# Optimization experiments

Measured on AMD Instinct MI355X. Metric: run time of the kernel, lower is better.

The kernel has to match this reference:

```python
import jax, jax.numpy as jnp
import numpy as np

B, N, M = 4, 2048, 2048
DIM, DIM_KEYS, DIM_OUT = 512, 512, 512
HEADS, DIM_HEAD = 8, 64
INNER = HEADS * DIM_HEAD


def setup_inputs() -> dict:
    key = jax.random.key(0)
    ks = jax.random.split(key, 9)
    x = jax.random.normal(ks[0], (B, N, DIM), dtype=jnp.float32)
    context = jax.random.normal(ks[1], (B, M, DIM_KEYS), dtype=jnp.float32)
    mask = jax.random.randint(ks[2], (B, N), 0, 2).astype(bool)
    context_mask = jax.random.randint(ks[3], (B, M), 0, 2).astype(bool)
    Wq = jax.random.normal(ks[4], (DIM, INNER), dtype=jnp.float32) * 0.02
    Wkv = jax.random.normal(ks[5], (DIM_KEYS, 2 * INNER), dtype=jnp.float32) * 0.02
    Wo = jax.random.normal(ks[6], (INNER, DIM_OUT), dtype=jnp.float32) * 0.02
    bo = jnp.zeros((DIM_OUT,), dtype=jnp.float32)
    null_key = jax.random.normal(ks[7], (DIM_HEAD,), dtype=jnp.float32)
    null_value = jax.random.normal(ks[8], (DIM_HEAD,), dtype=jnp.float32)
    return {"x": x, "context": context, "mask": mask, "context_mask": context_mask,
            "Wq": Wq, "Wkv": Wkv, "Wo": Wo, "bo": bo,
            "null_key": null_key, "null_value": null_value}


def reference(x, context, mask, context_mask, Wq, Wkv, Wo, bo, null_key, null_value):
    b, n, _ = x.shape
    m = context.shape[1]
    h, dh = HEADS, DIM_HEAD
    scale = dh ** -0.5

    # projections -> [b, h, n, dh]
    q = (x @ Wq).reshape(b, n, h, dh).transpose(0, 2, 1, 3)
    kv = context @ Wkv  # [b, m, 2*inner]
    k, v = jnp.split(kv, 2, axis=-1)
    k = k.reshape(b, m, h, dh).transpose(0, 2, 1, 3)
    v = v.reshape(b, m, h, dh).transpose(0, 2, 1, 3)

    # prepend null key/value token -> j = m + 1
    nk = jnp.broadcast_to(null_key, (b, h, 1, dh))
    nv = jnp.broadcast_to(null_value, (b, h, 1, dh))
    k = jnp.concatenate([nk, k], axis=2)
    v = jnp.concatenate([nv, v], axis=2)

    # qk activation (tanh) BEFORE the dot product
    q = jnp.tanh(q)
    k = jnp.tanh(k)

    sim = jnp.einsum('bhid,bhjd->bhij', q, k) * scale  # [b,h,n,m+1]

    # null token is always attendable -> pad context mask with True
    cm = jnp.pad(context_mask, ((0, 0), (1, 0)), constant_values=True)
    full_mask = mask[:, None, :, None] & cm[:, None, None, :]
    neg = -jnp.finfo(sim.dtype).max
    sim = jnp.where(full_mask, sim, neg)

    attn = jax.nn.softmax(sim, axis=-1)
    out = jnp.einsum('bhij,bhjd->bhid', attn, v)
    out = out.transpose(0, 2, 1, 3).reshape(b, n, h * dh)
    return out @ Wo + bo
```

## Files before the change

kernel.cpp:

```cpp
#include <hip/hip_runtime.h>
#include <math.h>

#define BB 4
#define NN 2048
#define MM 2048
#define HEADS 8
#define DH 64

typedef _Float16 f16;
typedef _Float16 f16x4 __attribute__((ext_vector_type(4)));
typedef _Float16 f16x8 __attribute__((ext_vector_type(8)));
typedef float f32x4 __attribute__((ext_vector_type(4)));
typedef short bf16x8v __attribute__((ext_vector_type(8)));
typedef unsigned short ushort;

#define LOG2E 1.44269504088896f
#define QSCALE (0.125f * LOG2E)

#if __has_builtin(__builtin_amdgcn_exp2f)
#define EXP2(x) __builtin_amdgcn_exp2f(x)
#else
#define EXP2(x) exp2f(x)
#endif

__device__ __forceinline__ void bsplit(float v, ushort& h, ushort& l) {
    unsigned bits = __float_as_uint(v);
    float res = v - __uint_as_float(bits & 0xffff0000u);
    h = (ushort)(bits >> 16);
    l = (ushort)(__float_as_uint(res) >> 16);
}

__device__ __forceinline__ f16x4 pk4(float a, float b, float c, float d) {
#if __has_builtin(__builtin_amdgcn_cvt_pkrtz)
    auto t0 = __builtin_amdgcn_cvt_pkrtz(a, b);
    auto t1 = __builtin_amdgcn_cvt_pkrtz(c, d);
    f16x4 r;
    r[0] = t0[0]; r[1] = t0[1]; r[2] = t1[0]; r[3] = t1[1];
    return r;
#else
    f16x4 r = {(f16)a, (f16)b, (f16)c, (f16)d};
    return r;
#endif
}

__global__ void wsplit_k(const float* __restrict__ W, ushort* __restrict__ Th,
                         ushort* __restrict__ Tl, int K, int N)
{
    __shared__ ushort Sh[64][36], Sl[64][36];
    const int tid = threadIdx.x;
    const int k0 = blockIdx.x * 32, n0 = blockIdx.y * 64;
    const int kr = tid >> 3, nc = (tid & 7) * 8;
    float4 v0 = *(const float4*)(W + (size_t)(k0 + kr) * N + n0 + nc);
    float4 v1 = *(const float4*)(W + (size_t)(k0 + kr) * N + n0 + nc + 4);
    float e[8] = {v0.x, v0.y, v0.z, v0.w, v1.x, v1.y, v1.z, v1.w};
#pragma unroll
    for (int j = 0; j < 8; j++) {
        ushort h, l;
        bsplit(e[j], h, l);
        Sh[nc + j][kr] = h;
        Sl[nc + j][kr] = l;
    }
    __syncthreads();
    const int n = tid >> 2, kc = (tid & 3) * 8;
    *(uint4*)(Th + (size_t)(n0 + n) * K + k0 + kc) = *(const uint4*)(&Sh[n][kc]);
    *(uint4*)(Tl + (size_t)(n0 + n) * K + k0 + kc) = *(const uint4*)(&Sl[n][kc]);
}

__global__ void wtrans_k(const float* __restrict__ W, f16* __restrict__ T16,
                         int K, int N)
{
    __shared__ f16 Sh[64][36];
    const int tid = threadIdx.x;
    const int k0 = blockIdx.x * 32, n0 = blockIdx.y * 64;
    const int kr = tid >> 3, nc = (tid & 7) * 8;
    float4 v0 = *(const float4*)(W + (size_t)(k0 + kr) * N + n0 + nc);
    float4 v1 = *(const float4*)(W + (size_t)(k0 + kr) * N + n0 + nc + 4);
    float e[8] = {v0.x, v0.y, v0.z, v0.w, v1.x, v1.y, v1.z, v1.w};
#pragma unroll
    for (int j = 0; j < 8; j++) Sh[nc + j][kr] = (f16)e[j];
    __syncthreads();
    const int n = tid >> 2, kc = (tid & 3) * 8;
    *(uint4*)(T16 + (size_t)(n0 + n) * K + k0 + kc) = *(const uint4*)(&Sh[n][kc]);
}

template<int MODE>
__launch_bounds__(256)
__global__ void fgemm(const float* __restrict__ A, const f16* __restrict__ Bt,
                      f16* __restrict__ o16a, f16* __restrict__ o16b, int K)
{
    __shared__ f16 sA[128 * 36];
    __shared__ f16 sB[64 * 36];

    const int tid  = threadIdx.x;
    const int wave = tid >> 6, lane = tid & 63;
    const int l15  = lane & 15, quad = lane >> 4;
    const size_t r0 = (size_t)blockIdx.x * 128;
    const int c0 = blockIdx.y * 64;

    const int ar = tid >> 1;
    const int ac = (tid & 1) * 16;
    const int br = tid >> 2;
    const int bc = (tid & 3) * 8;

    f32x4 acc[2][4] = {};

    for (int k0 = 0; k0 < K; k0 += 32) {
        const float* ap = A + (r0 + ar) * K + k0 + ac;
        float4 a0 = *(const float4*)(ap + 0);
        float4 a1 = *(const float4*)(ap + 4);
        float4 a2 = *(const float4*)(ap + 8);
        float4 a3 = *(const float4*)(ap + 12);
        uint4  bv = *(const uint4*)(Bt + (size_t)(c0 + br) * K + k0 + bc);
        f16x8 pa0, pa1;
        pa0[0] = (f16)a0.x; pa0[1] = (f16)a0.y; pa0[2] = (f16)a0.z; pa0[3] = (f16)a0.w;
        pa0[4] = (f16)a1.x; pa0[5] = (f16)a1.y; pa0[6] = (f16)a1.z; pa0[7] = (f16)a1.w;
        pa1[0] = (f16)a2.x; pa1[1] = (f16)a2.y; pa1[2] = (f16)a2.z; pa1[3] = (f16)a2.w;
        pa1[4] = (f16)a3.x; pa1[5] = (f16)a3.y; pa1[6] = (f16)a3.z; pa1[7] = (f16)a3.w;
        __syncthreads();
        *(f16x8*)(sA + ar * 36 + ac)     = pa0;
        *(f16x8*)(sA + ar * 36 + ac + 8) = pa1;
        *(uint4*)(sB + br * 36 + bc)     = bv;
        __syncthreads();

        f16x8 a[2], b[4];
#pragma unroll
        for (int rt = 0; rt < 2; rt++)
            a[rt] = *(const f16x8*)(sA + (wave * 32 + rt * 16 + l15) * 36 + quad * 8);
#pragma unroll
        for (int ct = 0; ct < 4; ct++)
            b[ct] = *(const f16x8*)(sB + (ct * 16 + l15) * 36 + quad * 8);
#pragma unroll
        for (int rt = 0; rt < 2; rt++)
#pragma unroll
            for (int ct = 0; ct < 4; ct++)
                acc[rt][ct] = __builtin_amdgcn_mfma_f32_16x16x32_f16(
                    a[rt], b[ct], acc[rt][ct], 0, 0, 0);
    }

    const int b    = (int)(r0 >> 11);
    const int rloc = ((int)(r0 & 2047)) + wave * 32;

#pragma unroll
    for (int rt = 0; rt < 2; rt++)
#pragma unroll
        for (int ct = 0; ct < 4; ct++) {
            if (MODE == 0 || (MODE == 1 && blockIdx.y < 8)) {
                const int h = blockIdx.y & 7;
                const int d = ct * 16 + l15;
#pragma unroll
                for (int reg = 0; reg < 4; reg++) {
                    const int n = rloc + rt * 16 + quad * 4 + reg;
                    float v = tanhf(acc[rt][ct][reg]);
                    if (MODE == 0) v *= QSCALE;
                    o16a[(((size_t)b * 8 + h) * 2048 + n) * 64 + d] = (f16)v;
                }
            } else {
                const int h = blockIdx.y - 8;
                const int d = ct * 16 + l15;
                const int m0 = rloc + rt * 16 + quad * 4;
                f16x4 pk;
#pragma unroll
                for (int reg = 0; reg < 4; reg++) pk[reg] = (f16)acc[rt][ct][reg];
                *(f16x4*)(o16b + (((size_t)b * 8 + h) * 64 + d) * 2048 + m0) = pk;
            }
        }
}

__launch_bounds__(256)
__global__ void attn_k(const f16* __restrict__ qws, const f16* __restrict__ kws,
                       const f16* __restrict__ vtws,
                       const int* __restrict__ mask, const int* __restrict__ cmask,
                       const float* __restrict__ nk, const float* __restrict__ nv,
                       ushort* __restrict__ oh, ushort* __restrict__ ol)
{
    __shared__ f16 sK[64 * 72];
    __shared__ f16 sV[64 * 72];

    const int tid  = threadIdx.x;
    const int wave = tid >> 6, lane = tid & 63;
    const int l15  = lane & 15, quad = lane >> 4;
    const int bh = blockIdx.x, b = bh >> 3, h = bh & 7;
    const int q0 = blockIdx.y * 64 + wave * 16;

    f16x8 qf[2];
    const f16* qbase = qws + ((size_t)bh * NN + q0) * DH;
#pragma unroll
    for (int ks = 0; ks < 2; ks++)
        qf[ks] = *(const f16x8*)(qbase + l15 * DH + ks * 32 + quad * 8);

    float pn = 0.f;
#pragma unroll
    for (int ks = 0; ks < 2; ks++)
#pragma unroll
        for (int t = 0; t < 8; t++)
            pn += (float)qf[ks][t] * tanhf(nk[ks * 32 + quad * 8 + t]);
    pn += __shfl_xor(pn, 16);
    pn += __shfl_xor(pn, 32);

    const int rowOk = mask[(size_t)b * NN + q0 + l15];
    const float pnull  = rowOk ? EXP2(pn) : 1.0f;
    const float negsel = rowOk ? -1.0e30f : 0.0f;
    if (!rowOk) {
        const f16x8 zz = {(f16)0, (f16)0, (f16)0, (f16)0, (f16)0, (f16)0, (f16)0, (f16)0};
        qf[0] = zz; qf[1] = zz;
    }

    f32x4 acc[4];
    f32x4 accl;
#pragma unroll
    for (int reg = 0; reg < 4; reg++) {
        const float pr = __shfl(pnull, quad * 4 + reg, 16);
        accl[reg] = pr;
#pragma unroll
        for (int ds = 0; ds < 4; ds++)
            acc[ds][reg] = pr * nv[ds * 16 + l15];
    }

    const f16* kg0 = kws + (size_t)bh * MM * DH;
    const f16* vg0 = vtws + (size_t)bh * DH * MM;
    const int sr = tid >> 2;
    const int sc = (tid & 3) * 16;
    const f16x4 vone = {(f16)1, (f16)1, (f16)1, (f16)1};

    for (int jc = 0; jc < MM; jc += 64) {
        uint4 kr0 = *(const uint4*)(kg0 + (size_t)(jc + sr) * DH + sc);
        uint4 kr1 = *(const uint4*)(kg0 + (size_t)(jc + sr) * DH + sc + 8);
        uint4 vr0 = *(const uint4*)(vg0 + (size_t)sr * MM + jc + sc);
        uint4 vr1 = *(const uint4*)(vg0 + (size_t)sr * MM + jc + sc + 8);
        int4 cmv[4];
#pragma unroll
        for (int jj = 0; jj < 4; jj++)
            cmv[jj] = *(const int4*)(cmask + (size_t)b * MM + jc + jj * 16 + quad * 4);

        __syncthreads();
        *(uint4*)(sK + sr * 72 + sc)     = kr0;
        *(uint4*)(sK + sr * 72 + sc + 8) = kr1;
        *(uint4*)(sV + sr * 72 + sc)     = vr0;
        *(uint4*)(sV + sr * 72 + sc + 8) = vr1;
        __syncthreads();

        f32x4 st[4];
#pragma unroll
        for (int jj = 0; jj < 4; jj++) {
            st[jj][0] = cmv[jj].x ? 0.0f : negsel;
            st[jj][1] = cmv[jj].y ? 0.0f : negsel;
            st[jj][2] = cmv[jj].z ? 0.0f : negsel;
            st[jj][3] = cmv[jj].w ? 0.0f : negsel;
        }

#pragma unroll
        for (int ks = 0; ks < 2; ks++) {
#pragma unroll
            for (int jj = 0; jj < 4; jj++) {
                f16x8 kb = *(const f16x8*)(sK + (jj * 16 + l15) * 72 + ks * 32 + quad * 8);
                st[jj] = __builtin_amdgcn_mfma_f32_16x16x32_f16(kb, qf[ks], st[jj], 0, 0, 0);
            }
        }

        f16x4 pa[4];
#pragma unroll
        for (int jj = 0; jj < 4; jj++)
            pa[jj] = pk4(EXP2(st[jj][0]), EXP2(st[jj][1]),
                         EXP2(st[jj][2]), EXP2(st[jj][3]));

#pragma unroll
        for (int jj = 0; jj < 4; jj++) {
#pragma unroll
            for (int ds = 0; ds < 4; ds++) {
                f16x4 vb = *(const f16x4*)(sV + (ds * 16 + l15) * 72 + jj * 16 + quad * 4);
                acc[ds] = __builtin_amdgcn_mfma_f32_16x16x16f16(pa[jj], vb, acc[ds], 0, 0, 0);
            }
            accl = __builtin_amdgcn_mfma_f32_16x16x16f16(pa[jj], vone, accl, 0, 0, 0);
        }
    }

    float inv[4];
#pragma unroll
    for (int reg = 0; reg < 4; reg++) inv[reg] = 1.0f / accl[reg];
#pragma unroll
    for (int ds = 0; ds < 4; ds++)
#pragma unroll
        for (int reg = 0; reg < 4; reg++) {
            const int r = q0 + quad * 4 + reg;
            float v = acc[ds][reg] * inv[reg];
            ushort hh, ll;
            bsplit(v, hh, ll);
            size_t idx = ((size_t)(b * 2048 + r)) * 512 + h * 64 + ds * 16 + l15;
            oh[idx] = hh;
            ol[idx] = ll;
        }
}

__launch_bounds__(256)
__global__ void mgemm2(const ushort* __restrict__ Ah, const ushort* __restrict__ Al,
                       const ushort* __restrict__ Bh, const ushort* __restrict__ Bl,
                       float* __restrict__ o32, const float* __restrict__ bias,
                       int K)
{
    __shared__ ushort sAh[128 * 36], sAl[128 * 36];
    __shared__ ushort sBh[64 * 36],  sBl[64 * 36];

    const int tid  = threadIdx.x;
    const int wave = tid >> 6, lane = tid & 63;
    const int l15  = lane & 15, quad = lane >> 4;
    const size_t r0 = (size_t)blockIdx.x * 128;
    const int c0 = blockIdx.y * 64;

    const int sr = tid >> 2;
    const int sc = (tid & 3) * 8;

    f32x4 acc[2][4] = {};

    for (int k0 = 0; k0 < K; k0 += 32) {
        uint4 ah0 = *(const uint4*)(Ah + (r0 + sr) * K + k0 + sc);
        uint4 ah1 = *(const uint4*)(Ah + (r0 + 64 + sr) * K + k0 + sc);
        uint4 al0 = *(const uint4*)(Al + (r0 + sr) * K + k0 + sc);
        uint4 al1 = *(const uint4*)(Al + (r0 + 64 + sr) * K + k0 + sc);
        uint4 bh  = *(const uint4*)(Bh + (size_t)(c0 + sr) * K + k0 + sc);
        uint4 bl  = *(const uint4*)(Bl + (size_t)(c0 + sr) * K + k0 + sc);
        __syncthreads();
        *(uint4*)(sAh + sr * 36 + sc)        = ah0;
        *(uint4*)(sAh + (64 + sr) * 36 + sc) = ah1;
        *(uint4*)(sAl + sr * 36 + sc)        = al0;
        *(uint4*)(sAl + (64 + sr) * 36 + sc) = al1;
        *(uint4*)(sBh + sr * 36 + sc)        = bh;
        *(uint4*)(sBl + sr * 36 + sc)        = bl;
        __syncthreads();

        bf16x8v a_h[2], a_l[2], b_h[4], b_l[4];
#pragma unroll
        for (int rt = 0; rt < 2; rt++) {
            const int r = wave * 32 + rt * 16 + l15;
            a_h[rt] = *(const bf16x8v*)(sAh + r * 36 + quad * 8);
            a_l[rt] = *(const bf16x8v*)(sAl + r * 36 + quad * 8);
        }
#pragma unroll
        for (int ct = 0; ct < 4; ct++) {
            const int c = ct * 16 + l15;
            b_h[ct] = *(const bf16x8v*)(sBh + c * 36 + quad * 8);
            b_l[ct] = *(const bf16x8v*)(sBl + c * 36 + quad * 8);
        }
#pragma unroll
        for (int rt = 0; rt < 2; rt++)
#pragma unroll
            for (int ct = 0; ct < 4; ct++) {
                acc[rt][ct] = __builtin_amdgcn_mfma_f32_16x16x32_bf16(a_h[rt], b_h[ct], acc[rt][ct], 0, 0, 0);
                acc[rt][ct] = __builtin_amdgcn_mfma_f32_16x16x32_bf16(a_h[rt], b_l[ct], acc[rt][ct], 0, 0, 0);
                acc[rt][ct] = __builtin_amdgcn_mfma_f32_16x16x32_bf16(a_l[rt], b_h[ct], acc[rt][ct], 0, 0, 0);
            }
    }

#pragma unroll
    for (int rt = 0; rt < 2; rt++)
#pragma unroll
        for (int ct = 0; ct < 4; ct++) {
            const int col = c0 + ct * 16 + l15;
            const float bv = bias[col];
#pragma unroll
            for (int reg = 0; reg < 4; reg++) {
                const size_t row = r0 + wave * 32 + rt * 16 + quad * 4 + reg;
                o32[row * 512 + col] = acc[rt][ct][reg] + bv;
            }
        }
}

extern "C" void kernel_launch(void* const* d_in, const int* in_sizes, int n_in,
                              void* d_out, int out_size, void* d_ws, size_t ws_size,
                              hipStream_t stream)
{
    const float* x    = (const float*)d_in[0];
    const float* ctx  = (const float*)d_in[1];
    const int*   mask = (const int*)d_in[2];
    const int*   cmsk = (const int*)d_in[3];
    const float* Wq   = (const float*)d_in[4];
    const float* Wkv  = (const float*)d_in[5];
    const float* Wo   = (const float*)d_in[6];
    const float* bo   = (const float*)d_in[7];
    const float* nk   = (const float*)d_in[8];
    const float* nv   = (const float*)d_in[9];
    float* out = (float*)d_out;

    const size_t S = (size_t)BB * HEADS * NN * DH;

    f16* qws = (f16*)d_ws;
    f16* kws = qws + S;
    f16* vt  = kws + S;
    ushort* oh = (ushort*)(vt + S);
    ushort* ol = oh + S;
    f16* wq16  = (f16*)(ol + S);
    f16* wkv16 = wq16 + 512 * 512;
    ushort* woh = (ushort*)(wkv16 + 512 * 1024);
    ushort* wol = woh + 512 * 512;

    wtrans_k<<<dim3(16, 8),  256, 0, stream>>>(Wq,  wq16,  512, 512);
    wtrans_k<<<dim3(16, 16), 256, 0, stream>>>(Wkv, wkv16, 512, 1024);
    wsplit_k<<<dim3(16, 8),  256, 0, stream>>>(Wo,  woh, wol, 512, 512);
    fgemm<0><<<dim3(64, 8),  256, 0, stream>>>(x,   wq16,  qws, nullptr, 512);
    fgemm<1><<<dim3(64, 16), 256, 0, stream>>>(ctx, wkv16, kws, vt,      512);
    attn_k<<<dim3(32, 32), 256, 0, stream>>>(qws, kws, vt, mask, cmsk, nk, nv, oh, ol);
    mgemm2<<<dim3(64, 8),  256, 0, stream>>>(oh, ol, woh, wol, out, bo, 512);
}
```

Baseline: 226.5 us.

## Split attention KV range across two blocks with merge kernel; fuse prep and projection launches

The attention kernel now splits the key range into two halves along a new grid dimension, writing unnormalised fp32 partial outputs and row sums that a new merge kernel combines, normalises and splits into hi/lo bf16. The aim is to double the block count for better occupancy and latency hiding. The three weight-prep kernels and the two projection GEMMs are also each fused into single launches to cut launch overhead. The cost is an extra fp32 partial-output round trip through memory and an added kernel; workspace is reused by aliasing the hi/lo output buffers onto the q/k buffers.

```diff
diff --git a/kernel.cpp b/kernel.cpp
--- a/kernel.cpp
+++ b/kernel.cpp
@@ -43,50 +43,49 @@
 #endif
 }
 
-__global__ void wsplit_k(const float* __restrict__ W, ushort* __restrict__ Th,
-                         ushort* __restrict__ Tl, int K, int N)
-{
-    __shared__ ushort Sh[64][36], Sl[64][36];
+__global__ void wprep_k(const float* __restrict__ Wq, const float* __restrict__ Wkv,
+                        const float* __restrict__ Wo,
+                        f16* __restrict__ wq16, f16* __restrict__ wkv16,
+                        ushort* __restrict__ woh, ushort* __restrict__ wol)
+{
+    __shared__ ushort S0[64 * 36], S1[64 * 36];
     const int tid = threadIdx.x;
-    const int k0 = blockIdx.x * 32, n0 = blockIdx.y * 64;
+    const int bid = blockIdx.x;
+    const int K = 512;
+    const float* W; int N; f16* T16; ushort *Th, *Tl; int id;
+    if (bid < 128)      { W = Wq;  N = 512;  T16 = wq16;  Th = 0; Tl = 0; id = bid; }
+    else if (bid < 384) { W = Wkv; N = 1024; T16 = wkv16; Th = 0; Tl = 0; id = bid - 128; }
+    else                { W = Wo;  N = 512;  T16 = 0; Th = woh; Tl = wol; id = bid - 384; }
+    const int k0 = (id & 15) * 32, n0 = (id >> 4) * 64;
     const int kr = tid >> 3, nc = (tid & 7) * 8;
     float4 v0 = *(const float4*)(W + (size_t)(k0 + kr) * N + n0 + nc);
     float4 v1 = *(const float4*)(W + (size_t)(k0 + kr) * N + n0 + nc + 4);
     float e[8] = {v0.x, v0.y, v0.z, v0.w, v1.x, v1.y, v1.z, v1.w};
-#pragma unroll
-    for (int j = 0; j < 8; j++) {
-        ushort h, l;
-        bsplit(e[j], h, l);
-        Sh[nc + j][kr] = h;
-        Sl[nc + j][kr] = l;
-    }
-    __syncthreads();
     const int n = tid >> 2, kc = (tid & 3) * 8;
-    *(uint4*)(Th + (size_t)(n0 + n) * K + k0 + kc) = *(const uint4*)(&Sh[n][kc]);
-    *(uint4*)(Tl + (size_t)(n0 + n) * K + k0 + kc) = *(const uint4*)(&Sl[n][kc]);
-}
-
-__global__ void wtrans_k(const float* __restrict__ W, f16* __restrict__ T16,
-                         int K, int N)
-{
-    __shared__ f16 Sh[64][36];
-    const int tid = threadIdx.x;
-    const int k0 = blockIdx.x * 32, n0 = blockIdx.y * 64;
-    const int kr = tid >> 3, nc = (tid & 7) * 8;
-    float4 v0 = *(const float4*)(W + (size_t)(k0 + kr) * N + n0 + nc);
-    float4 v1 = *(const float4*)(W + (size_t)(k0 + kr) * N + n0 + nc + 4);
-    float e[8] = {v0.x, v0.y, v0.z, v0.w, v1.x, v1.y, v1.z, v1.w};
-#pragma unroll
-    for (int j = 0; j < 8; j++) Sh[nc + j][kr] = (f16)e[j];
-    __syncthreads();
-    const int n = tid >> 2, kc = (tid & 3) * 8;
-    *(uint4*)(T16 + (size_t)(n0 + n) * K + k0 + kc) = *(const uint4*)(&Sh[n][kc]);
-}
-
-template<int MODE>
+    if (T16) {
+        f16* Sf = (f16*)S0;
+#pragma unroll
+        for (int j = 0; j < 8; j++) Sf[(nc + j) * 36 + kr] = (f16)e[j];
+        __syncthreads();
+        *(uint4*)(T16 + (size_t)(n0 + n) * K + k0 + kc) = *(const uint4*)(Sf + n * 36 + kc);
+    } else {
+#pragma unroll
+        for (int j = 0; j < 8; j++) {
+            ushort h, l;
+            bsplit(e[j], h, l);
+            S0[(nc + j) * 36 + kr] = h;
+            S1[(nc + j) * 36 + kr] = l;
+        }
+        __syncthreads();
+        *(uint4*)(Th + (size_t)(n0 + n) * K + k0 + kc) = *(const uint4*)(S0 + n * 36 + kc);
+        *(uint4*)(Tl + (size_t)(n0 + n) * K + k0 + kc) = *(const uint4*)(S1 + n * 36 + kc);
+    }
+}
+
 __launch_bounds__(256)
-__global__ void fgemm(const float* __restrict__ A, const f16* __restrict__ Bt,
-                      f16* __restrict__ o16a, f16* __restrict__ o16b, int K)
+__global__ void proj_k(const float* __restrict__ x, const float* __restrict__ ctx,
+                       const f16* __restrict__ wq16, const f16* __restrict__ wkv16,
+                       f16* __restrict__ qws, f16* __restrict__ kws, f16* __restrict__ vt)
 {
     __shared__ f16 sA[128 * 36];
     __shared__ f16 sB[64 * 36];
@@ -94,8 +93,13 @@
     const int tid  = threadIdx.x;
     const int wave = tid >> 6, lane = tid & 63;
     const int l15  = lane & 15, quad = lane >> 4;
+    const int by = blockIdx.y;
+    const int isQ = (by < 8);
+    const float* A = isQ ? x : ctx;
+    const f16* Bt  = isQ ? wq16 : wkv16;
+    const int c0 = (isQ ? by : by - 8) * 64;
     const size_t r0 = (size_t)blockIdx.x * 128;
-    const int c0 = blockIdx.y * 64;
+    const int K = 512;
 
     const int ar = tid >> 1;
     const int ac = (tid & 1) * 16;
@@ -144,24 +148,25 @@
     for (int rt = 0; rt < 2; rt++)
 #pragma unroll
         for (int ct = 0; ct < 4; ct++) {
-            if (MODE == 0 || (MODE == 1 && blockIdx.y < 8)) {
-                const int h = blockIdx.y & 7;
+            if (by < 16) {
+                const int h = by & 7;
                 const int d = ct * 16 + l15;
+                f16* dst = isQ ? qws : kws;
+                const float sc = isQ ? QSCALE : 1.0f;
 #pragma unroll
                 for (int reg = 0; reg < 4; reg++) {
-                    const int n = rloc + rt * 16 + quad * 4 + reg;
-                    float v = tanhf(acc[rt][ct][reg]);
-                    if (MODE == 0) v *= QSCALE;
-                    o16a[(((size_t)b * 8 + h) * 2048 + n) * 64 + d] = (f16)v;
+                    const int nn = rloc + rt * 16 + quad * 4 + reg;
+                    dst[(((size_t)b * 8 + h) * 2048 + nn) * 64 + d] =
+                        (f16)(tanhf(acc[rt][ct][reg]) * sc);
                 }
             } else {
-                const int h = blockIdx.y - 8;
+                const int h = by - 16;
                 const int d = ct * 16 + l15;
                 const int m0 = rloc + rt * 16 + quad * 4;
                 f16x4 pk;
 #pragma unroll
                 for (int reg = 0; reg < 4; reg++) pk[reg] = (f16)acc[rt][ct][reg];
-                *(f16x4*)(o16b + (((size_t)b * 8 + h) * 64 + d) * 2048 + m0) = pk;
+                *(f16x4*)(vt + (((size_t)b * 8 + h) * 64 + d) * 2048 + m0) = pk;
             }
         }
 }
@@ -171,7 +176,7 @@
                        const f16* __restrict__ vtws,
                        const int* __restrict__ mask, const int* __restrict__ cmask,
                        const float* __restrict__ nk, const float* __restrict__ nv,
-                       ushort* __restrict__ oh, ushort* __restrict__ ol)
+                       float* __restrict__ Op, float* __restrict__ lp)
 {
     __shared__ f16 sK[64 * 72];
     __shared__ f16 sV[64 * 72];
@@ -181,6 +186,7 @@
     const int l15  = lane & 15, quad = lane >> 4;
     const int bh = blockIdx.x, b = bh >> 3, h = bh & 7;
     const int q0 = blockIdx.y * 64 + wave * 16;
+    const int jh = blockIdx.z;
 
     f16x8 qf[2];
     const f16* qbase = qws + ((size_t)bh * NN + q0) * DH;
@@ -188,18 +194,21 @@
     for (int ks = 0; ks < 2; ks++)
         qf[ks] = *(const f16x8*)(qbase + l15 * DH + ks * 32 + quad * 8);
 
-    float pn = 0.f;
-#pragma unroll
-    for (int ks = 0; ks < 2; ks++)
-#pragma unroll
-        for (int t = 0; t < 8; t++)
-            pn += (float)qf[ks][t] * tanhf(nk[ks * 32 + quad * 8 + t]);
-    pn += __shfl_xor(pn, 16);
-    pn += __shfl_xor(pn, 32);
-
     const int rowOk = mask[(size_t)b * NN + q0 + l15];
-    const float pnull  = rowOk ? EXP2(pn) : 1.0f;
     const float negsel = rowOk ? -1.0e30f : 0.0f;
+
+    float pnull = 0.0f;
+    if (jh == 0) {
+        float pn = 0.f;
+#pragma unroll
+        for (int ks = 0; ks < 2; ks++)
+#pragma unroll
+            for (int t = 0; t < 8; t++)
+                pn += (float)qf[ks][t] * tanhf(nk[ks * 32 + quad * 8 + t]);
+        pn += __shfl_xor(pn, 16);
+        pn += __shfl_xor(pn, 32);
+        pnull = rowOk ? EXP2(pn) : 1.0f;
+    }
     if (!rowOk) {
         const f16x8 zz = {(f16)0, (f16)0, (f16)0, (f16)0, (f16)0, (f16)0, (f16)0, (f16)0};
         qf[0] = zz; qf[1] = zz;
@@ -221,8 +230,9 @@
     const int sr = tid >> 2;
     const int sc = (tid & 3) * 16;
     const f16x4 vone = {(f16)1, (f16)1, (f16)1, (f16)1};
-
-    for (int jc = 0; jc < MM; jc += 64) {
+    const int jbeg = jh << 10, jend = jbeg + 1024;
+
+    for (int jc = jbeg; jc < jend; jc += 64) {
         uint4 kr0 = *(const uint4*)(kg0 + (size_t)(jc + sr) * DH + sc);
         uint4 kr1 = *(const uint4*)(kg0 + (size_t)(jc + sr) * DH + sc + 8);
         uint4 vr0 = *(const uint4*)(vg0 + (size_t)sr * MM + jc + sc);
@@ -274,21 +284,42 @@
         }
     }
 
-    float inv[4];
-#pragma unroll
-    for (int reg = 0; reg < 4; reg++) inv[reg] = 1.0f / accl[reg];
 #pragma unroll
     for (int ds = 0; ds < 4; ds++)
 #pragma unroll
         for (int reg = 0; reg < 4; reg++) {
             const int r = q0 + quad * 4 + reg;
-            float v = acc[ds][reg] * inv[reg];
-            ushort hh, ll;
-            bsplit(v, hh, ll);
-            size_t idx = ((size_t)(b * 2048 + r)) * 512 + h * 64 + ds * 16 + l15;
-            oh[idx] = hh;
-            ol[idx] = ll;
-        }
+            Op[((size_t)jh * 8192 + b * 2048 + r) * 512 + h * 64 + ds * 16 + l15] =
+                acc[ds][reg];
+        }
+    if (l15 == 0) {
+#pragma unroll
+        for (int reg = 0; reg < 4; reg++)
+            lp[((size_t)jh * 32 + bh) * 2048 + q0 + quad * 4 + reg] = accl[reg];
+    }
+}
+
+__global__ void merge_k(const float* __restrict__ Op, const float* __restrict__ lp,
+                        ushort* __restrict__ oh, ushort* __restrict__ ol)
+{
+    const int i = blockIdx.x * 256 + threadIdx.x;
+    const int row = i >> 7;
+    const int c4  = i & 127;
+    const int b = row >> 11, n = row & 2047, h = c4 >> 4;
+    const float l = lp[((size_t)b * 8 + h) * 2048 + n] +
+                    lp[((size_t)32 + b * 8 + h) * 2048 + n];
+    const float inv = 1.0f / l;
+    const float4 o1 = *(const float4*)(Op + (size_t)row * 512 + c4 * 4);
+    const float4 o2 = *(const float4*)(Op + (size_t)(8192 + row) * 512 + c4 * 4);
+    float v[4] = {(o1.x + o2.x) * inv, (o1.y + o2.y) * inv,
+                  (o1.z + o2.z) * inv, (o1.w + o2.w) * inv};
+    ushort hh[4], ll[4];
+#pragma unroll
+    for (int j = 0; j < 4; j++) bsplit(v[j], hh[j], ll[j]);
+    ushort4 H = {hh[0], hh[1], hh[2], hh[3]};
+    ushort4 L = {ll[0], ll[1], ll[2], ll[3]};
+    *(ushort4*)(oh + (size_t)row * 512 + c4 * 4) = H;
+    *(ushort4*)(ol + (size_t)row * 512 + c4 * 4) = L;
 }
 
 __launch_bounds__(256)
@@ -385,18 +416,18 @@
     f16* qws = (f16*)d_ws;
     f16* kws = qws + S;
     f16* vt  = kws + S;
-    ushort* oh = (ushort*)(vt + S);
-    ushort* ol = oh + S;
-    f16* wq16  = (f16*)(ol + S);
+    f16* wq16  = vt + S;
     f16* wkv16 = wq16 + 512 * 512;
     ushort* woh = (ushort*)(wkv16 + 512 * 1024);
     ushort* wol = woh + 512 * 512;
-
-    wtrans_k<<<dim3(16, 8),  256, 0, stream>>>(Wq,  wq16,  512, 512);
-    wtrans_k<<<dim3(16, 16), 256, 0, stream>>>(Wkv, wkv16, 512, 1024);
-    wsplit_k<<<dim3(16, 8),  256, 0, stream>>>(Wo,  woh, wol, 512, 512);
-    fgemm<0><<<dim3(64, 8),  256, 0, stream>>>(x,   wq16,  qws, nullptr, 512);
-    fgemm<1><<<dim3(64, 16), 256, 0, stream>>>(ctx, wkv16, kws, vt,      512);
-    attn_k<<<dim3(32, 32), 256, 0, stream>>>(qws, kws, vt, mask, cmsk, nk, nv, oh, ol);
-    mgemm2<<<dim3(64, 8),  256, 0, stream>>>(oh, ol, woh, wol, out, bo, 512);
-}
+    float* lp = (float*)(wol + 512 * 512);
+    float* Op = lp + 2 * 32 * 2048;
+    ushort* oh = (ushort*)qws;
+    ushort* ol = (ushort*)kws;
+
+    wprep_k<<<512, 256, 0, stream>>>(Wq, Wkv, Wo, wq16, wkv16, woh, wol);
+    proj_k<<<dim3(64, 24), 256, 0, stream>>>(x, ctx, wq16, wkv16, qws, kws, vt);
+    attn_k<<<dim3(32, 32, 2), 256, 0, stream>>>(qws, kws, vt, mask, cmsk, nk, nv, Op, lp);
+    merge_k<<<4096, 256, 0, stream>>>(Op, lp, oh, ol);
+    mgemm2<<<dim3(64, 8), 256, 0, stream>>>(oh, ol, woh, wol, out, bo, 512);
+}
```

Result: no change. 222.8 us (-1.6%).
